# Kernel tuning notes

Measured on AMD Instinct MI355X. Metric: run time of the kernel, lower is better.

Reference implementation:

```python
import jax, jax.numpy as jnp
import numpy as np

NOT_EPSILON = 1.0
B, S, D = 1, 512, 256


def swishmax(x, axis):
    xexp = x * jnp.exp(x - jnp.max(x, axis=axis, keepdims=True))
    return xexp / (jnp.sum(jnp.abs(xexp), axis=axis, keepdims=True) + NOT_EPSILON)


def setup_inputs() -> dict:
    key = jax.random.key(0)
    ks = jax.random.split(key, 13)
    scale = 1.0 / np.sqrt(D)
    mk = lambda k: jax.random.uniform(k, (D, D), jnp.float32, -scale, scale)
    mb = lambda k: jax.random.uniform(k, (D,), jnp.float32, -scale, scale)
    return {
        "query_tokens": jax.random.normal(ks[0], (B, S, D), jnp.float32),
        "key_tokens": jax.random.normal(ks[1], (B, S, D), jnp.float32),
        "value_tokens": jax.random.normal(ks[2], (B, S, D), jnp.float32),
        "Wk": mk(ks[3]), "bk": mb(ks[4]),
        "Wq": mk(ks[5]), "bq": mb(ks[6]),
        "Wva": mk(ks[7]), "bva": mb(ks[8]),
        "Wl": mk(ks[9]), "bl": mb(ks[10]),
        "Wvo": mk(ks[11]), "bvo": mb(ks[12]),
    }


def reference(query_tokens, key_tokens, value_tokens,
              Wk, bk, Wq, bq, Wva, bva, Wl, bl, Wvo, bvo):
    # residual linear transforms of tokens
    k = key_tokens + key_tokens @ Wk + bk        # [B,S,D]
    q = query_tokens + query_tokens @ Wq + bq    # [B,S,D]
    # batchify: key -> [B,Sk,1,D], query -> [B,1,Sq,D]; outer-product scores
    attention_raw = k[:, :, None, :] * q[:, None, :, :]          # [B,Sk,Sq,D]
    attention_logits = attention_raw + attention_raw @ Wl + bl   # DxD linear on raw scores
    attention_scale = swishmax(attention_logits, axis=-2)        # normalize over query axis (dim -shape_dims)
    v = value_tokens + value_tokens @ Wva + bva  # [B,S,D]
    values_scaled = v[:, :, None, :] * attention_scale           # [B,Sk,Sq,D]
    value_sum = values_scaled.sum(axis=-3)                       # reduce key axis -> [B,Sq,D]
    value_out = value_sum + value_sum @ Wvo + bvo
    return value_out
```

## Files before the change

kernel.cpp:

```cpp
#include <hip/hip_runtime.h>
#include <math.h>

#define S_LEN 512
#define D_DIM 256
#define SLICE (S_LEN * D_DIM)

#define LOG2E  1.44269504088896f
#define LN2    0.69314718055995f
#define C2     (8.0f * LOG2E)

#define EXP2F(x) __builtin_amdgcn_exp2f(x)


typedef _Float16 half8  __attribute__((ext_vector_type(8)));
typedef _Float16 half4v __attribute__((ext_vector_type(4)));
typedef float   floatx4 __attribute__((ext_vector_type(4)));

__global__ __launch_bounds__(256) void linres3(
    const float* __restrict__ xk, const float* __restrict__ Wk,
    const float* __restrict__ bk, _Float16* __restrict__ yk16,
    const float* __restrict__ xq, const float* __restrict__ Wq,
    const float* __restrict__ bq, _Float16* __restrict__ yq16,
    const float* __restrict__ xv, const float* __restrict__ Wv,
    const float* __restrict__ bv, float* __restrict__ yv,
    const float* __restrict__ Wl, _Float16* __restrict__ WlhT)
{
    const int tid = threadIdx.x;
    const int sel = blockIdx.y;

    if (sel == 3) {
        #pragma unroll
        for (int t = 0; t < 2; ++t) {
            const int d = blockIdx.x * 2 + t;
            float v = (Wl[tid * D_DIM + d] + (tid == d ? 1.0f : 0.0f)) * LOG2E;
            WlhT[d * D_DIM + tid] = (_Float16)v;
        }
        return;
    }

    __shared__ float xs[4][D_DIM];
    const int r0 = blockIdx.x * 4;
    const float* x = sel == 0 ? xk : (sel == 1 ? xq : xv);
    const float* W = sel == 0 ? Wk : (sel == 1 ? Wq : Wv);
    const float* b = sel == 0 ? bk : (sel == 1 ? bq : bv);

    #pragma unroll
    for (int t = 0; t < 4; ++t) xs[t][tid] = x[(r0 + t) * D_DIM + tid];
    __syncthreads();
    const float bv_ = b[tid];
    float acc[4];
    #pragma unroll
    for (int i = 0; i < 4; ++i) acc[i] = xs[i][tid] + bv_;
    #pragma unroll 8
    for (int e = 0; e < D_DIM; ++e) {
        const float w = W[e * D_DIM + tid];
        #pragma unroll
        for (int i = 0; i < 4; ++i) acc[i] += xs[i][e] * w;
    }
    if (sel == 2) {
        #pragma unroll
        for (int i = 0; i < 4; ++i) yv[(r0 + i) * D_DIM + tid] = acc[i];
    } else {
        _Float16* y16 = sel == 0 ? yk16 : yq16;
        #pragma unroll
        for (int i = 0; i < 4; ++i) y16[(r0 + i) * D_DIM + tid] = (_Float16)acc[i];
    }
}

__global__ __launch_bounds__(256) void linres_sum(
    const float* __restrict__ po, const float* __restrict__ W,
    const float* __restrict__ b, float* __restrict__ y)
{
    __shared__ float xs[2][D_DIM];
    const int tid = threadIdx.x;
    const int r0  = blockIdx.x * 2;
    #pragma unroll
    for (int t = 0; t < 2; ++t) {
        float s = 0.f;
        #pragma unroll
        for (int c = 0; c < 16; ++c)
            s += po[(size_t)c * SLICE + (r0 + t) * D_DIM + tid];
        xs[t][tid] = s;
    }
    __syncthreads();
    const float bv_ = b[tid];
    float acc[2];
    #pragma unroll
    for (int i = 0; i < 2; ++i) acc[i] = xs[i][tid] + bv_;
    #pragma unroll 8
    for (int e = 0; e < D_DIM; ++e) {
        const float w = W[e * D_DIM + tid];
        #pragma unroll
        for (int i = 0; i < 2; ++i) acc[i] += xs[i][e] * w;
    }
    #pragma unroll
    for (int i = 0; i < 2; ++i) y[(r0 + i) * D_DIM + tid] = acc[i];
}

__device__ __forceinline__ void stage_q(const _Float16* __restrict__ qh,
                                        _Float16* __restrict__ Afrag,
                                        int sq0, int tid)
{
    const int i   = tid & 63;
    const int qtr = tid >> 6;
    const int mt = i >> 4, l16 = i & 15;
    const half8* src = (const half8*)(qh + (size_t)(sq0 + i) * D_DIM + qtr * 64);
    #pragma unroll
    for (int u = 0; u < 8; ++u) {
        const int eb   = qtr * 8 + u;
        const int kk   = eb >> 2, quad = eb & 3;
        const int addr16 = (mt * 8 + kk) * 64 + quad * 16 + l16;
        *(half8*)(Afrag + addr16 * 8) = src[u];
    }
}

__device__ __forceinline__ void stage_q32(const _Float16* __restrict__ qh,
                                          _Float16* __restrict__ Afrag,
                                          int sq0, int tid)
{
    const int i   = tid & 31;
    const int oct = tid >> 5;
    const int mt = i >> 4, l16 = i & 15;
    const half8* src = (const half8*)(qh + (size_t)(sq0 + i) * D_DIM);
    #pragma unroll
    for (int u = 0; u < 4; ++u) {
        const int eb   = oct * 4 + u;
        const int kk   = eb >> 2, quad = eb & 3;
        const int addr16 = (mt * 8 + kk) * 64 + quad * 16 + l16;
        *(half8*)(Afrag + addr16 * 8) = src[eb];
    }
}

__global__ __launch_bounds__(256, 2) void stats_mfma(
    const _Float16* __restrict__ qh, const _Float16* __restrict__ kh,
    const _Float16* __restrict__ WlhT, const float* __restrict__ bl,
    float* __restrict__ pm, float* __restrict__ ps)
{
    __shared__ _Float16 Afrag[32 * 64 * 8];

    const int tid  = threadIdx.x;
    const int lane = tid & 63, wave = tid >> 6;
    const int quad = lane >> 4, l16 = lane & 15;
    const int sqt  = blockIdx.x, sq0 = sqt * 64;
    const int dw   = blockIdx.y * 128 + wave * 32;
    const int sk0  = blockIdx.z * 16;

    stage_q(qh, Afrag, sq0, tid);

    half8 wl[2][8];
    #pragma unroll
    for (int nt = 0; nt < 2; ++nt) {
        const int d = dw + nt * 16 + l16;
        #pragma unroll
        for (int kk = 0; kk < 8; ++kk)
            wl[nt][kk] = *(const half8*)(WlhT + (size_t)d * D_DIM + kk * 32 + quad * 8);
    }
    float bl_r[2];
    #pragma unroll
    for (int nt = 0; nt < 2; ++nt)
        bl_r[nt] = bl[dw + nt * 16 + l16] * LOG2E;

    __syncthreads();

    #pragma unroll 1
    for (int s = 0; s < 16; ++s) {
        const int sk = sk0 + s;
        floatx4 acc[4][2];
        #pragma unroll
        for (int mt = 0; mt < 4; ++mt)
            #pragma unroll
            for (int nt = 0; nt < 2; ++nt)
                acc[mt][nt] = (floatx4){0.f, 0.f, 0.f, 0.f};

        #pragma unroll
        for (int kk = 0; kk < 8; ++kk) {
            const half8 k8 = *(const half8*)(kh + (size_t)sk * D_DIM + kk * 32 + quad * 8);
            half8 af[4], bf[2];
            #pragma unroll
            for (int mt = 0; mt < 4; ++mt)
                af[mt] = *(const half8*)(Afrag + ((mt * 8 + kk) * 64 + lane) * 8);
            #pragma unroll
            for (int nt = 0; nt < 2; ++nt)
                bf[nt] = wl[nt][kk] * k8;
            #pragma unroll
            for (int mt = 0; mt < 4; ++mt)
                #pragma unroll
                for (int nt = 0; nt < 2; ++nt)
                    acc[mt][nt] = __builtin_amdgcn_mfma_f32_16x16x32_f16(
                        af[mt], bf[nt], acc[mt][nt], 0, 0, 0);
        }

        #pragma unroll
        for (int nt = 0; nt < 2; ++nt) {
            float mmx[4], tss[4];
            #pragma unroll
            for (int mt = 0; mt < 4; ++mt) {
                float L0 = acc[mt][nt][0] + bl_r[nt];
                float L1 = acc[mt][nt][1] + bl_r[nt];
                float L2 = acc[mt][nt][2] + bl_r[nt];
                float L3 = acc[mt][nt][3] + bl_r[nt];
                float t0 = fabsf(L0) * EXP2F(L0 - C2);
                float t1 = fabsf(L1) * EXP2F(L1 - C2);
                float t2 = fabsf(L2) * EXP2F(L2 - C2);
                float t3 = fabsf(L3) * EXP2F(L3 - C2);
                mmx[mt] = fmaxf(fmaxf(L0, L1), fmaxf(L2, L3));
                tss[mt] = (t0 + t1) + (t2 + t3);
            }
            float m  = fmaxf(fmaxf(mmx[0], mmx[1]), fmaxf(mmx[2], mmx[3]));
            float ss = (tss[0] + tss[1]) + (tss[2] + tss[3]);

            #pragma unroll
            for (int mask = 16; mask <= 32; mask <<= 1) {
                m  = fmaxf(m, __shfl_xor(m, mask, 64));
                ss += __shfl_xor(ss, mask, 64);
            }
            if (quad == 0) {
                const int d = dw + nt * 16 + l16;
                pm[((size_t)sqt * S_LEN + sk) * D_DIM + d] = m;
                ps[((size_t)sqt * S_LEN + sk) * D_DIM + d] = ss;
            }
        }
    }
}

__global__ __launch_bounds__(256) void reduce_ms(
    const float* __restrict__ pm, const float* __restrict__ ps,
    const float* __restrict__ vbuf, float* __restrict__ wbuf)
{
    const int idx = blockIdx.x * 256 + threadIdx.x;
    float mv[8], sv[8];
    #pragma unroll
    for (int t = 0; t < 8; ++t) {
        mv[t] = pm[(size_t)t * SLICE + idx];
        sv[t] = ps[(size_t)t * SLICE + idx];
    }
    float M = fmaxf(fmaxf(fmaxf(mv[0], mv[1]), fmaxf(mv[2], mv[3])),
                    fmaxf(fmaxf(mv[4], mv[5]), fmaxf(mv[6], mv[7])));
    float S = ((sv[0] + sv[1]) + (sv[2] + sv[3]))
            + ((sv[4] + sv[5]) + (sv[6] + sv[7]));
    const float denom = S * LN2 + EXP2F(M - C2);
    wbuf[idx] = vbuf[idx] * (LN2 / denom);
}

__global__ __launch_bounds__(256)
__attribute__((amdgpu_waves_per_eu(2, 2)))
void accum_mfma(
    const _Float16* __restrict__ qh, const _Float16* __restrict__ kh,
    const _Float16* __restrict__ WlhT, const float* __restrict__ bl,
    const float* __restrict__ wbuf, float* __restrict__ po)
{
    __shared__ _Float16 Afrag[16 * 64 * 8];

    const int tid  = threadIdx.x;
    const int lane = tid & 63, wave = tid >> 6;
    const int quad = lane >> 4, l16 = lane & 15;
    const int sq0  = blockIdx.x * 32;
    const int dw   = blockIdx.y * 128 + wave * 32;
    const int chunk = blockIdx.z;
    const int sk0  = chunk * 32;

    stage_q32(qh, Afrag, sq0, tid);

    half8 wl[2][8];
    #pragma unroll
    for (int nt = 0; nt < 2; ++nt) {
        const int d = dw + nt * 16 + l16;
        #pragma unroll
        for (int kk = 0; kk < 8; ++kk)
            wl[nt][kk] = *(const half8*)(WlhT + (size_t)d * D_DIM + kk * 32 + quad * 8);
    }
    float bl_r[2];
    #pragma unroll
    for (int nt = 0; nt < 2; ++nt)
        bl_r[nt] = bl[dw + nt * 16 + l16] * LOG2E;

    __syncthreads();

    half8 afr[2][8];
    #pragma unroll
    for (int mt = 0; mt < 2; ++mt)
        #pragma unroll
        for (int kk = 0; kk < 8; ++kk)
            afr[mt][kk] = *(const half8*)(Afrag + ((mt * 8 + kk) * 64 + lane) * 8);

    floatx4 o[2][2];
    #pragma unroll
    for (int mt = 0; mt < 2; ++mt)
        #pragma unroll
        for (int nt = 0; nt < 2; ++nt)
            o[mt][nt] = (floatx4){0.f, 0.f, 0.f, 0.f};

    half8 k8c[8];
    #pragma unroll
    for (int kk = 0; kk < 8; ++kk)
        k8c[kk] = *(const half8*)(kh + (size_t)sk0 * D_DIM + kk * 32 + quad * 8);
    float w_c0 = wbuf[(size_t)sk0 * D_DIM + dw + l16];
    float w_c1 = wbuf[(size_t)sk0 * D_DIM + dw + 16 + l16];

    #pragma unroll 1
    for (int s = 0; s < 32; ++s) {
        const int sk = sk0 + s;

        floatx4 acc[2][2];
        #pragma unroll
        for (int mt = 0; mt < 2; ++mt)
            #pragma unroll
            for (int nt = 0; nt < 2; ++nt)
                acc[mt][nt] = (floatx4){0.f, 0.f, 0.f, 0.f};

        #pragma unroll
        for (int kk = 0; kk < 8; ++kk) {
            const half8 bf0 = wl[0][kk] * k8c[kk];
            const half8 bf1 = wl[1][kk] * k8c[kk];
            acc[0][0] = __builtin_amdgcn_mfma_f32_16x16x32_f16(afr[0][kk], bf0, acc[0][0], 0, 0, 0);
            acc[0][1] = __builtin_amdgcn_mfma_f32_16x16x32_f16(afr[0][kk], bf1, acc[0][1], 0, 0, 0);
            acc[1][0] = __builtin_amdgcn_mfma_f32_16x16x32_f16(afr[1][kk], bf0, acc[1][0], 0, 0, 0);
            acc[1][1] = __builtin_amdgcn_mfma_f32_16x16x32_f16(afr[1][kk], bf1, acc[1][1], 0, 0, 0);
        }

        const float w_use0 = w_c0, w_use1 = w_c1;
        if (s < 31) {
            #pragma unroll
            for (int kk = 0; kk < 8; ++kk)
                k8c[kk] = *(const half8*)(kh + (size_t)(sk + 1) * D_DIM + kk * 32 + quad * 8);
            w_c0 = wbuf[(size_t)(sk + 1) * D_DIM + dw + l16];
            w_c1 = wbuf[(size_t)(sk + 1) * D_DIM + dw + 16 + l16];
        }

        #pragma unroll
        for (int mt = 0; mt < 2; ++mt)
            #pragma unroll
            for (int r = 0; r < 4; ++r) {
                const float La = acc[mt][0][r] + bl_r[0];
                const float Lb = acc[mt][1][r] + bl_r[1];
                o[mt][0][r] += w_use0 * (La * EXP2F(La - C2));
                o[mt][1][r] += w_use1 * (Lb * EXP2F(Lb - C2));
            }
    }

    float* dst = po + (size_t)chunk * SLICE;
    #pragma unroll
    for (int mt = 0; mt < 2; ++mt)
        #pragma unroll
        for (int nt = 0; nt < 2; ++nt)
            #pragma unroll
            for (int r = 0; r < 4; ++r) {
                const int row = sq0 + mt * 16 + quad * 4 + r;
                const int col = dw + nt * 16 + l16;
                dst[(size_t)row * D_DIM + col] = o[mt][nt][r];
            }
}

extern "C" void kernel_launch(void* const* d_in, const int* in_sizes, int n_in,
                              void* d_out, int out_size, void* d_ws, size_t ws_size,
                              hipStream_t stream)
{
    const float* query = (const float*)d_in[0];
    const float* key   = (const float*)d_in[1];
    const float* value = (const float*)d_in[2];
    const float* Wk  = (const float*)d_in[3];
    const float* bk  = (const float*)d_in[4];
    const float* Wq  = (const float*)d_in[5];
    const float* bq  = (const float*)d_in[6];
    const float* Wva = (const float*)d_in[7];
    const float* bva = (const float*)d_in[8];
    const float* Wl  = (const float*)d_in[9];
    const float* bl  = (const float*)d_in[10];
    const float* Wvo = (const float*)d_in[11];
    const float* bvo = (const float*)d_in[12];

    const int MAT = SLICE;
    float* ws   = (float*)d_ws;
    float* vbuf = ws + 2 * MAT;
    float* wbuf = ws + 3 * MAT;
    _Float16* WlhT = (_Float16*)(ws + 6 * MAT);
    _Float16* kh   = (_Float16*)(ws + 6 * MAT + 32768);
    _Float16* qh   = kh + MAT;
    float* pm  = ws + 6 * MAT + 32768 + 2 * 65536;
    float* ps  = pm + 8 * MAT;
    float* po  = pm;
    float* out = (float*)d_out;

    linres3<<<dim3(128, 4), 256, 0, stream>>>(key, Wk, bk, kh,
                                              query, Wq, bq, qh,
                                              value, Wva, bva, vbuf,
                                              Wl, WlhT);

    stats_mfma<<<dim3(8, 2, 32), 256, 0, stream>>>(qh, kh, WlhT, bl, pm, ps);
    reduce_ms<<<512, 256, 0, stream>>>(pm, ps, vbuf, wbuf);
    accum_mfma<<<dim3(16, 2, 16), 256, 0, stream>>>(qh, kh, WlhT, bl,
                                                    wbuf, po);

    linres_sum<<<256, 256, 0, stream>>>(po, Wvo, bvo, out);
}
```

Measured before the change: 194.5 us.

## Fuse all five kernels into one persistent kernel with grid barriers

Replaces the five separate launches (linear projections, stats, reduce, accumulate, output projection) with a single 512-block kernel that runs each phase in turn and separates them with a software grid-wide barrier built on atomics. The aim is to remove per-launch overhead and the gaps between kernels. The price is that every phase must now use 512 blocks, the shared-memory buffer is the largest one needed by any phase, and the final projection is done one row per block. All 512 blocks must be resident at once or the barrier deadlocks, and barrier spinning adds its own latency.

```diff
diff --git a/kernel.cpp b/kernel.cpp
--- a/kernel.cpp
+++ b/kernel.cpp
@@ -4,6 +4,7 @@
 #define S_LEN 512
 #define D_DIM 256
 #define SLICE (S_LEN * D_DIM)
+#define NBLK  512
 
 #define LOG2E  1.44269504088896f
 #define LN2    0.69314718055995f
@@ -13,342 +14,346 @@
 
 
 typedef _Float16 half8  __attribute__((ext_vector_type(8)));
-typedef _Float16 half4v __attribute__((ext_vector_type(4)));
 typedef float   floatx4 __attribute__((ext_vector_type(4)));
 
-__global__ __launch_bounds__(256) void linres3(
-    const float* __restrict__ xk, const float* __restrict__ Wk,
-    const float* __restrict__ bk, _Float16* __restrict__ yk16,
-    const float* __restrict__ xq, const float* __restrict__ Wq,
-    const float* __restrict__ bq, _Float16* __restrict__ yq16,
-    const float* __restrict__ xv, const float* __restrict__ Wv,
-    const float* __restrict__ bv, float* __restrict__ yv,
-    const float* __restrict__ Wl, _Float16* __restrict__ WlhT)
+__device__ __forceinline__ void grid_barrier(int* bar)
 {
-    const int tid = threadIdx.x;
-    const int sel = blockIdx.y;
-
-    if (sel == 3) {
-        #pragma unroll
-        for (int t = 0; t < 2; ++t) {
-            const int d = blockIdx.x * 2 + t;
-            float v = (Wl[tid * D_DIM + d] + (tid == d ? 1.0f : 0.0f)) * LOG2E;
-            WlhT[d * D_DIM + tid] = (_Float16)v;
-        }
-        return;
-    }
-
-    __shared__ float xs[4][D_DIM];
-    const int r0 = blockIdx.x * 4;
-    const float* x = sel == 0 ? xk : (sel == 1 ? xq : xv);
-    const float* W = sel == 0 ? Wk : (sel == 1 ? Wq : Wv);
-    const float* b = sel == 0 ? bk : (sel == 1 ? bq : bv);
-
-    #pragma unroll
-    for (int t = 0; t < 4; ++t) xs[t][tid] = x[(r0 + t) * D_DIM + tid];
     __syncthreads();
-    const float bv_ = b[tid];
-    float acc[4];
-    #pragma unroll
-    for (int i = 0; i < 4; ++i) acc[i] = xs[i][tid] + bv_;
-    #pragma unroll 8
-    for (int e = 0; e < D_DIM; ++e) {
-        const float w = W[e * D_DIM + tid];
-        #pragma unroll
-        for (int i = 0; i < 4; ++i) acc[i] += xs[i][e] * w;
-    }
-    if (sel == 2) {
-        #pragma unroll
-        for (int i = 0; i < 4; ++i) yv[(r0 + i) * D_DIM + tid] = acc[i];
-    } else {
-        _Float16* y16 = sel == 0 ? yk16 : yq16;
-        #pragma unroll
-        for (int i = 0; i < 4; ++i) y16[(r0 + i) * D_DIM + tid] = (_Float16)acc[i];
-    }
+    if (threadIdx.x == 0) {
+        __threadfence();
+        int* cnt = bar;
+        int* gen = bar + 1;
+        const int g = __hip_atomic_load(gen, __ATOMIC_RELAXED,
+                                        __HIP_MEMORY_SCOPE_AGENT);
+        const int prev = __hip_atomic_fetch_add(cnt, 1, __ATOMIC_ACQ_REL,
+                                                __HIP_MEMORY_SCOPE_AGENT);
+        if (prev == NBLK - 1) {
+            __hip_atomic_store(cnt, 0, __ATOMIC_RELAXED,
+                               __HIP_MEMORY_SCOPE_AGENT);
+            __hip_atomic_fetch_add(gen, 1, __ATOMIC_RELEASE,
+                                   __HIP_MEMORY_SCOPE_AGENT);
+        } else {
+            while (__hip_atomic_load(gen, __ATOMIC_RELAXED,
+                                     __HIP_MEMORY_SCOPE_AGENT) == g)
+                __builtin_amdgcn_s_sleep(8);
+        }
+        __threadfence();
+    }
+    __syncthreads();
 }
 
-__global__ __launch_bounds__(256) void linres_sum(
-    const float* __restrict__ po, const float* __restrict__ W,
-    const float* __restrict__ b, float* __restrict__ y)
+__global__ __launch_bounds__(256)
+__attribute__((amdgpu_waves_per_eu(2, 2)))
+void fused_all(
+    const float* __restrict__ query, const float* __restrict__ key,
+    const float* __restrict__ value,
+    const float* __restrict__ Wk,  const float* __restrict__ bk,
+    const float* __restrict__ Wq,  const float* __restrict__ bq,
+    const float* __restrict__ Wva, const float* __restrict__ bva,
+    const float* __restrict__ Wl,  const float* __restrict__ bl,
+    const float* __restrict__ Wvo, const float* __restrict__ bvo,
+    _Float16* __restrict__ kh, _Float16* __restrict__ qh,
+    float* __restrict__ vbuf, _Float16* __restrict__ WlhT,
+    float* __restrict__ pm, float* __restrict__ ps,
+    float* __restrict__ wbuf, float* __restrict__ po,
+    float* __restrict__ out, int* bar)
 {
-    __shared__ float xs[2][D_DIM];
-    const int tid = threadIdx.x;
-    const int r0  = blockIdx.x * 2;
-    #pragma unroll
-    for (int t = 0; t < 2; ++t) {
-        float s = 0.f;
-        #pragma unroll
-        for (int c = 0; c < 16; ++c)
-            s += po[(size_t)c * SLICE + (r0 + t) * D_DIM + tid];
-        xs[t][tid] = s;
-    }
-    __syncthreads();
-    const float bv_ = b[tid];
-    float acc[2];
-    #pragma unroll
-    for (int i = 0; i < 2; ++i) acc[i] = xs[i][tid] + bv_;
-    #pragma unroll 8
-    for (int e = 0; e < D_DIM; ++e) {
-        const float w = W[e * D_DIM + tid];
-        #pragma unroll
-        for (int i = 0; i < 2; ++i) acc[i] += xs[i][e] * w;
-    }
-    #pragma unroll
-    for (int i = 0; i < 2; ++i) y[(r0 + i) * D_DIM + tid] = acc[i];
-}
-
-__device__ __forceinline__ void stage_q(const _Float16* __restrict__ qh,
-                                        _Float16* __restrict__ Afrag,
-                                        int sq0, int tid)
-{
-    const int i   = tid & 63;
-    const int qtr = tid >> 6;
-    const int mt = i >> 4, l16 = i & 15;
-    const half8* src = (const half8*)(qh + (size_t)(sq0 + i) * D_DIM + qtr * 64);
-    #pragma unroll
-    for (int u = 0; u < 8; ++u) {
-        const int eb   = qtr * 8 + u;
-        const int kk   = eb >> 2, quad = eb & 3;
-        const int addr16 = (mt * 8 + kk) * 64 + quad * 16 + l16;
-        *(half8*)(Afrag + addr16 * 8) = src[u];
-    }
-}
-
-__device__ __forceinline__ void stage_q32(const _Float16* __restrict__ qh,
-                                          _Float16* __restrict__ Afrag,
-                                          int sq0, int tid)
-{
-    const int i   = tid & 31;
-    const int oct = tid >> 5;
-    const int mt = i >> 4, l16 = i & 15;
-    const half8* src = (const half8*)(qh + (size_t)(sq0 + i) * D_DIM);
-    #pragma unroll
-    for (int u = 0; u < 4; ++u) {
-        const int eb   = oct * 4 + u;
-        const int kk   = eb >> 2, quad = eb & 3;
-        const int addr16 = (mt * 8 + kk) * 64 + quad * 16 + l16;
-        *(half8*)(Afrag + addr16 * 8) = src[eb];
-    }
-}
-
-__global__ __launch_bounds__(256, 2) void stats_mfma(
-    const _Float16* __restrict__ qh, const _Float16* __restrict__ kh,
-    const _Float16* __restrict__ WlhT, const float* __restrict__ bl,
-    float* __restrict__ pm, float* __restrict__ ps)
-{
-    __shared__ _Float16 Afrag[32 * 64 * 8];
+    __shared__ __align__(16) _Float16 AfragS[32 * 64 * 8];
 
     const int tid  = threadIdx.x;
+    const int bid  = blockIdx.x;
     const int lane = tid & 63, wave = tid >> 6;
     const int quad = lane >> 4, l16 = lane & 15;
-    const int sqt  = blockIdx.x, sq0 = sqt * 64;
-    const int dw   = blockIdx.y * 128 + wave * 32;
-    const int sk0  = blockIdx.z * 16;
-
-    stage_q(qh, Afrag, sq0, tid);
-
-    half8 wl[2][8];
-    #pragma unroll
-    for (int nt = 0; nt < 2; ++nt) {
-        const int d = dw + nt * 16 + l16;
+
+    {
+        const int sel = bid >> 7;
+        const int bx  = bid & 127;
+        if (sel == 3) {
+            #pragma unroll
+            for (int t = 0; t < 2; ++t) {
+                const int d = bx * 2 + t;
+                float v = (Wl[tid * D_DIM + d] + (tid == d ? 1.0f : 0.0f)) * LOG2E;
+                WlhT[d * D_DIM + tid] = (_Float16)v;
+            }
+        } else {
+            float* xsf = (float*)AfragS;
+            const int r0 = bx * 4;
+            const float* x = sel == 0 ? key : (sel == 1 ? query : value);
+            const float* W = sel == 0 ? Wk : (sel == 1 ? Wq : Wva);
+            const float* b = sel == 0 ? bk : (sel == 1 ? bq : bva);
+
+            #pragma unroll
+            for (int t = 0; t < 4; ++t)
+                xsf[t * D_DIM + tid] = x[(r0 + t) * D_DIM + tid];
+            __syncthreads();
+            const float bv_ = b[tid];
+            float acc[4];
+            #pragma unroll
+            for (int i = 0; i < 4; ++i) acc[i] = xsf[i * D_DIM + tid] + bv_;
+            #pragma unroll 8
+            for (int e = 0; e < D_DIM; ++e) {
+                const float w = W[e * D_DIM + tid];
+                #pragma unroll
+                for (int i = 0; i < 4; ++i) acc[i] += xsf[i * D_DIM + e] * w;
+            }
+            if (sel == 2) {
+                #pragma unroll
+                for (int i = 0; i < 4; ++i) vbuf[(r0 + i) * D_DIM + tid] = acc[i];
+            } else {
+                _Float16* y16 = sel == 0 ? kh : qh;
+                #pragma unroll
+                for (int i = 0; i < 4; ++i)
+                    y16[(r0 + i) * D_DIM + tid] = (_Float16)acc[i];
+            }
+        }
+    }
+    grid_barrier(bar);
+
+    {
+        _Float16* Afrag = AfragS;
+        const int sqt = bid & 7,  sq0 = sqt * 64;
+        const int by  = (bid >> 3) & 1;
+        const int bz  = bid >> 4;
+        const int dw  = by * 128 + wave * 32;
+        const int sk0 = bz * 16;
+
+        {
+            const int i   = tid & 63;
+            const int qtr = tid >> 6;
+            const int mt = i >> 4, sl16 = i & 15;
+            const half8* src = (const half8*)(qh + (size_t)(sq0 + i) * D_DIM + qtr * 64);
+            #pragma unroll
+            for (int u = 0; u < 8; ++u) {
+                const int eb = qtr * 8 + u;
+                const int kk = eb >> 2, q4 = eb & 3;
+                const int addr16 = (mt * 8 + kk) * 64 + q4 * 16 + sl16;
+                *(half8*)(Afrag + addr16 * 8) = src[u];
+            }
+        }
+
+        half8 wl[2][8];
+        #pragma unroll
+        for (int nt = 0; nt < 2; ++nt) {
+            const int d = dw + nt * 16 + l16;
+            #pragma unroll
+            for (int kk = 0; kk < 8; ++kk)
+                wl[nt][kk] = *(const half8*)(WlhT + (size_t)d * D_DIM + kk * 32 + quad * 8);
+        }
+        float bl_r[2];
+        #pragma unroll
+        for (int nt = 0; nt < 2; ++nt)
+            bl_r[nt] = bl[dw + nt * 16 + l16] * LOG2E;
+
+        __syncthreads();
+
+        #pragma unroll 1
+        for (int s = 0; s < 16; ++s) {
+            const int sk = sk0 + s;
+            floatx4 acc[4][2];
+            #pragma unroll
+            for (int mt = 0; mt < 4; ++mt)
+                #pragma unroll
+                for (int nt = 0; nt < 2; ++nt)
+                    acc[mt][nt] = (floatx4){0.f, 0.f, 0.f, 0.f};
+
+            #pragma unroll
+            for (int kk = 0; kk < 8; ++kk) {
+                const half8 k8 = *(const half8*)(kh + (size_t)sk * D_DIM + kk * 32 + quad * 8);
+                half8 af[4], bf[2];
+                #pragma unroll
+                for (int mt = 0; mt < 4; ++mt)
+                    af[mt] = *(const half8*)(Afrag + ((mt * 8 + kk) * 64 + lane) * 8);
+                #pragma unroll
+                for (int nt = 0; nt < 2; ++nt)
+                    bf[nt] = wl[nt][kk] * k8;
+                #pragma unroll
+                for (int mt = 0; mt < 4; ++mt)
+                    #pragma unroll
+                    for (int nt = 0; nt < 2; ++nt)
+                        acc[mt][nt] = __builtin_amdgcn_mfma_f32_16x16x32_f16(
+                            af[mt], bf[nt], acc[mt][nt], 0, 0, 0);
+            }
+
+            #pragma unroll
+            for (int nt = 0; nt < 2; ++nt) {
+                float mmx[4], tss[4];
+                #pragma unroll
+                for (int mt = 0; mt < 4; ++mt) {
+                    float L0 = acc[mt][nt][0] + bl_r[nt];
+                    float L1 = acc[mt][nt][1] + bl_r[nt];
+                    float L2 = acc[mt][nt][2] + bl_r[nt];
+                    float L3 = acc[mt][nt][3] + bl_r[nt];
+                    float t0 = fabsf(L0) * EXP2F(L0 - C2);
+                    float t1 = fabsf(L1) * EXP2F(L1 - C2);
+                    float t2 = fabsf(L2) * EXP2F(L2 - C2);
+                    float t3 = fabsf(L3) * EXP2F(L3 - C2);
+                    mmx[mt] = fmaxf(fmaxf(L0, L1), fmaxf(L2, L3));
+                    tss[mt] = (t0 + t1) + (t2 + t3);
+                }
+                float m  = fmaxf(fmaxf(mmx[0], mmx[1]), fmaxf(mmx[2], mmx[3]));
+                float ss = (tss[0] + tss[1]) + (tss[2] + tss[3]);
+
+                #pragma unroll
+                for (int mask = 16; mask <= 32; mask <<= 1) {
+                    m  = fmaxf(m, __shfl_xor(m, mask, 64));
+                    ss += __shfl_xor(ss, mask, 64);
+                }
+                if (quad == 0) {
+                    const int d = dw + nt * 16 + l16;
+                    pm[((size_t)sqt * S_LEN + sk) * D_DIM + d] = m;
+                    ps[((size_t)sqt * S_LEN + sk) * D_DIM + d] = ss;
+                }
+            }
+        }
+    }
+    grid_barrier(bar);
+
+    {
+        const int idx = bid * 256 + tid;
+        float mv[8], sv[8];
+        #pragma unroll
+        for (int t = 0; t < 8; ++t) {
+            mv[t] = pm[(size_t)t * SLICE + idx];
+            sv[t] = ps[(size_t)t * SLICE + idx];
+        }
+        float M = fmaxf(fmaxf(fmaxf(mv[0], mv[1]), fmaxf(mv[2], mv[3])),
+                        fmaxf(fmaxf(mv[4], mv[5]), fmaxf(mv[6], mv[7])));
+        float S = ((sv[0] + sv[1]) + (sv[2] + sv[3]))
+                + ((sv[4] + sv[5]) + (sv[6] + sv[7]));
+        const float denom = S * LN2 + EXP2F(M - C2);
+        wbuf[idx] = vbuf[idx] * (LN2 / denom);
+    }
+    grid_barrier(bar);
+
+    {
+        _Float16* Afrag = AfragS;
+        const int bx = bid & 15;
+        const int by = (bid >> 4) & 1;
+        const int chunk = bid >> 5;
+        const int sq0 = bx * 32;
+        const int dw  = by * 128 + wave * 32;
+        const int sk0 = chunk * 32;
+
+        {
+            const int i   = tid & 31;
+            const int oct = tid >> 5;
+            const int mt = i >> 4, sl16 = i & 15;
+            const half8* src = (const half8*)(qh + (size_t)(sq0 + i) * D_DIM);
+            #pragma unroll
+            for (int u = 0; u < 4; ++u) {
+                const int eb = oct * 4 + u;
+                const int kk = eb >> 2, q4 = eb & 3;
+                const int addr16 = (mt * 8 + kk) * 64 + q4 * 16 + sl16;
+                *(half8*)(Afrag + addr16 * 8) = src[eb];
+            }
+        }
+
+        half8 wl[2][8];
+        #pragma unroll
+        for (int nt = 0; nt < 2; ++nt) {
+            const int d = dw + nt * 16 + l16;
+            #pragma unroll
+            for (int kk = 0; kk < 8; ++kk)
+                wl[nt][kk] = *(const half8*)(WlhT + (size_t)d * D_DIM + kk * 32 + quad * 8);
+        }
+        float bl_r[2];
+        #pragma unroll
+        for (int nt = 0; nt < 2; ++nt)
+            bl_r[nt] = bl[dw + nt * 16 + l16] * LOG2E;
+
+        __syncthreads();
+
+        half8 afr[2][8];
+        #pragma unroll
+        for (int mt = 0; mt < 2; ++mt)
+            #pragma unroll
+            for (int kk = 0; kk < 8; ++kk)
+                afr[mt][kk] = *(const half8*)(Afrag + ((mt * 8 + kk) * 64 + lane) * 8);
+
+        floatx4 o[2][2];
+        #pragma unroll
+        for (int mt = 0; mt < 2; ++mt)
+            #pragma unroll
+            for (int nt = 0; nt < 2; ++nt)
+                o[mt][nt] = (floatx4){0.f, 0.f, 0.f, 0.f};
+
+        half8 k8c[8];
         #pragma unroll
         for (int kk = 0; kk < 8; ++kk)
-            wl[nt][kk] = *(const half8*)(WlhT + (size_t)d * D_DIM + kk * 32 + quad * 8);
-    }
-    float bl_r[2];
-    #pragma unroll
-    for (int nt = 0; nt < 2; ++nt)
-        bl_r[nt] = bl[dw + nt * 16 + l16] * LOG2E;
-
-    __syncthreads();
-
-    #pragma unroll 1
-    for (int s = 0; s < 16; ++s) {
-        const int sk = sk0 + s;
-        floatx4 acc[4][2];
-        #pragma unroll
-        for (int mt = 0; mt < 4; ++mt)
+            k8c[kk] = *(const half8*)(kh + (size_t)sk0 * D_DIM + kk * 32 + quad * 8);
+        float w_c0 = wbuf[(size_t)sk0 * D_DIM + dw + l16];
+        float w_c1 = wbuf[(size_t)sk0 * D_DIM + dw + 16 + l16];
+
+        #pragma unroll 1
+        for (int s = 0; s < 32; ++s) {
+            const int sk = sk0 + s;
+
+            floatx4 acc[2][2];
+            #pragma unroll
+            for (int mt = 0; mt < 2; ++mt)
+                #pragma unroll
+                for (int nt = 0; nt < 2; ++nt)
+                    acc[mt][nt] = (floatx4){0.f, 0.f, 0.f, 0.f};
+
+            #pragma unroll
+            for (int kk = 0; kk < 8; ++kk) {
+                const half8 bf0 = wl[0][kk] * k8c[kk];
+                const half8 bf1 = wl[1][kk] * k8c[kk];
+                acc[0][0] = __builtin_amdgcn_mfma_f32_16x16x32_f16(afr[0][kk], bf0, acc[0][0], 0, 0, 0);
+                acc[0][1] = __builtin_amdgcn_mfma_f32_16x16x32_f16(afr[0][kk], bf1, acc[0][1], 0, 0, 0);
+                acc[1][0] = __builtin_amdgcn_mfma_f32_16x16x32_f16(afr[1][kk], bf0, acc[1][0], 0, 0, 0);
+                acc[1][1] = __builtin_amdgcn_mfma_f32_16x16x32_f16(afr[1][kk], bf1, acc[1][1], 0, 0, 0);
+            }
+
+            const float w_use0 = w_c0, w_use1 = w_c1;
+            if (s < 31) {
+                #pragma unroll
+                for (int kk = 0; kk < 8; ++kk)
+                    k8c[kk] = *(const half8*)(kh + (size_t)(sk + 1) * D_DIM + kk * 32 + quad * 8);
+                w_c0 = wbuf[(size_t)(sk + 1) * D_DIM + dw + l16];
+                w_c1 = wbuf[(size_t)(sk + 1) * D_DIM + dw + 16 + l16];
+            }
+
+            #pragma unroll
+            for (int mt = 0; mt < 2; ++mt)
+                #pragma unroll
+                for (int r = 0; r < 4; ++r) {
+                    const float La = acc[mt][0][r] + bl_r[0];
+                    const float Lb = acc[mt][1][r] + bl_r[1];
+                    o[mt][0][r] += w_use0 * (La * EXP2F(La - C2));
+                    o[mt][1][r] += w_use1 * (Lb * EXP2F(Lb - C2));
+                }
+        }
+
+        float* dst = po + (size_t)chunk * SLICE;
+        #pragma unroll
+        for (int mt = 0; mt < 2; ++mt)
             #pragma unroll
             for (int nt = 0; nt < 2; ++nt)
-                acc[mt][nt] = (floatx4){0.f, 0.f, 0.f, 0.f};
-
-        #pragma unroll
-        for (int kk = 0; kk < 8; ++kk) {
-            const half8 k8 = *(const half8*)(kh + (size_t)sk * D_DIM + kk * 32 + quad * 8);
-            half8 af[4], bf[2];
-            #pragma unroll
-            for (int mt = 0; mt < 4; ++mt)
-                af[mt] = *(const half8*)(Afrag + ((mt * 8 + kk) * 64 + lane) * 8);
-            #pragma unroll
-            for (int nt = 0; nt < 2; ++nt)
-                bf[nt] = wl[nt][kk] * k8;
-            #pragma unroll
-            for (int mt = 0; mt < 4; ++mt)
-                #pragma unroll
-                for (int nt = 0; nt < 2; ++nt)
-                    acc[mt][nt] = __builtin_amdgcn_mfma_f32_16x16x32_f16(
-                        af[mt], bf[nt], acc[mt][nt], 0, 0, 0);
-        }
-
-        #pragma unroll
-        for (int nt = 0; nt < 2; ++nt) {
-            float mmx[4], tss[4];
-            #pragma unroll
-            for (int mt = 0; mt < 4; ++mt) {
-                float L0 = acc[mt][nt][0] + bl_r[nt];
-                float L1 = acc[mt][nt][1] + bl_r[nt];
-                float L2 = acc[mt][nt][2] + bl_r[nt];
-                float L3 = acc[mt][nt][3] + bl_r[nt];
-                float t0 = fabsf(L0) * EXP2F(L0 - C2);
-                float t1 = fabsf(L1) * EXP2F(L1 - C2);
-                float t2 = fabsf(L2) * EXP2F(L2 - C2);
-                float t3 = fabsf(L3) * EXP2F(L3 - C2);
-                mmx[mt] = fmaxf(fmaxf(L0, L1), fmaxf(L2, L3));
-                tss[mt] = (t0 + t1) + (t2 + t3);
-            }
-            float m  = fmaxf(fmaxf(mmx[0], mmx[1]), fmaxf(mmx[2], mmx[3]));
-            float ss = (tss[0] + tss[1]) + (tss[2] + tss[3]);
-
-            #pragma unroll
-            for (int mask = 16; mask <= 32; mask <<= 1) {
-                m  = fmaxf(m, __shfl_xor(m, mask, 64));
-                ss += __shfl_xor(ss, mask, 64);
-            }
-            if (quad == 0) {
-                const int d = dw + nt * 16 + l16;
-                pm[((size_t)sqt * S_LEN + sk) * D_DIM + d] = m;
-                ps[((size_t)sqt * S_LEN + sk) * D_DIM + d] = ss;
-            }
-        }
-    }
-}
-
-__global__ __launch_bounds__(256) void reduce_ms(
-    const float* __restrict__ pm, const float* __restrict__ ps,
-    const float* __restrict__ vbuf, float* __restrict__ wbuf)
-{
-    const int idx = blockIdx.x * 256 + threadIdx.x;
-    float mv[8], sv[8];
-    #pragma unroll
-    for (int t = 0; t < 8; ++t) {
-        mv[t] = pm[(size_t)t * SLICE + idx];
-        sv[t] = ps[(size_t)t * SLICE + idx];
-    }
-    float M = fmaxf(fmaxf(fmaxf(mv[0], mv[1]), fmaxf(mv[2], mv[3])),
-                    fmaxf(fmaxf(mv[4], mv[5]), fmaxf(mv[6], mv[7])));
-    float S = ((sv[0] + sv[1]) + (sv[2] + sv[3]))
-            + ((sv[4] + sv[5]) + (sv[6] + sv[7]));
-    const float denom = S * LN2 + EXP2F(M - C2);
-    wbuf[idx] = vbuf[idx] * (LN2 / denom);
-}
-
-__global__ __launch_bounds__(256)
-__attribute__((amdgpu_waves_per_eu(2, 2)))
-void accum_mfma(
-    const _Float16* __restrict__ qh, const _Float16* __restrict__ kh,
-    const _Float16* __restrict__ WlhT, const float* __restrict__ bl,
-    const float* __restrict__ wbuf, float* __restrict__ po)
-{
-    __shared__ _Float16 Afrag[16 * 64 * 8];
-
-    const int tid  = threadIdx.x;
-    const int lane = tid & 63, wave = tid >> 6;
-    const int quad = lane >> 4, l16 = lane & 15;
-    const int sq0  = blockIdx.x * 32;
-    const int dw   = blockIdx.y * 128 + wave * 32;
-    const int chunk = blockIdx.z;
-    const int sk0  = chunk * 32;
-
-    stage_q32(qh, Afrag, sq0, tid);
-
-    half8 wl[2][8];
-    #pragma unroll
-    for (int nt = 0; nt < 2; ++nt) {
-        const int d = dw + nt * 16 + l16;
-        #pragma unroll
-        for (int kk = 0; kk < 8; ++kk)
-            wl[nt][kk] = *(const half8*)(WlhT + (size_t)d * D_DIM + kk * 32 + quad * 8);
-    }
-    float bl_r[2];
-    #pragma unroll
-    for (int nt = 0; nt < 2; ++nt)
-        bl_r[nt] = bl[dw + nt * 16 + l16] * LOG2E;
-
-    __syncthreads();
-
-    half8 afr[2][8];
-    #pragma unroll
-    for (int mt = 0; mt < 2; ++mt)
-        #pragma unroll
-        for (int kk = 0; kk < 8; ++kk)
-            afr[mt][kk] = *(const half8*)(Afrag + ((mt * 8 + kk) * 64 + lane) * 8);
-
-    floatx4 o[2][2];
-    #pragma unroll
-    for (int mt = 0; mt < 2; ++mt)
-        #pragma unroll
-        for (int nt = 0; nt < 2; ++nt)
-            o[mt][nt] = (floatx4){0.f, 0.f, 0.f, 0.f};
-
-    half8 k8c[8];
-    #pragma unroll
-    for (int kk = 0; kk < 8; ++kk)
-        k8c[kk] = *(const half8*)(kh + (size_t)sk0 * D_DIM + kk * 32 + quad * 8);
-    float w_c0 = wbuf[(size_t)sk0 * D_DIM + dw + l16];
-    float w_c1 = wbuf[(size_t)sk0 * D_DIM + dw + 16 + l16];
-
-    #pragma unroll 1
-    for (int s = 0; s < 32; ++s) {
-        const int sk = sk0 + s;
-
-        floatx4 acc[2][2];
-        #pragma unroll
-        for (int mt = 0; mt < 2; ++mt)
-            #pragma unroll
-            for (int nt = 0; nt < 2; ++nt)
-                acc[mt][nt] = (floatx4){0.f, 0.f, 0.f, 0.f};
-
-        #pragma unroll
-        for (int kk = 0; kk < 8; ++kk) {
-            const half8 bf0 = wl[0][kk] * k8c[kk];
-            const half8 bf1 = wl[1][kk] * k8c[kk];
-            acc[0][0] = __builtin_amdgcn_mfma_f32_16x16x32_f16(afr[0][kk], bf0, acc[0][0], 0, 0, 0);
-            acc[0][1] = __builtin_amdgcn_mfma_f32_16x16x32_f16(afr[0][kk], bf1, acc[0][1], 0, 0, 0);
-            acc[1][0] = __builtin_amdgcn_mfma_f32_16x16x32_f16(afr[1][kk], bf0, acc[1][0], 0, 0, 0);
-            acc[1][1] = __builtin_amdgcn_mfma_f32_16x16x32_f16(afr[1][kk], bf1, acc[1][1], 0, 0, 0);
-        }
-
-        const float w_use0 = w_c0, w_use1 = w_c1;
-        if (s < 31) {
-            #pragma unroll
-            for (int kk = 0; kk < 8; ++kk)
-                k8c[kk] = *(const half8*)(kh + (size_t)(sk + 1) * D_DIM + kk * 32 + quad * 8);
-            w_c0 = wbuf[(size_t)(sk + 1) * D_DIM + dw + l16];
-            w_c1 = wbuf[(size_t)(sk + 1) * D_DIM + dw + 16 + l16];
-        }
-
-        #pragma unroll
-        for (int mt = 0; mt < 2; ++mt)
-            #pragma unroll
-            for (int r = 0; r < 4; ++r) {
-                const float La = acc[mt][0][r] + bl_r[0];
-                const float Lb = acc[mt][1][r] + bl_r[1];
-                o[mt][0][r] += w_use0 * (La * EXP2F(La - C2));
-                o[mt][1][r] += w_use1 * (Lb * EXP2F(Lb - C2));
-            }
-    }
-
-    float* dst = po + (size_t)chunk * SLICE;
-    #pragma unroll
-    for (int mt = 0; mt < 2; ++mt)
-        #pragma unroll
-        for (int nt = 0; nt < 2; ++nt)
-            #pragma unroll
-            for (int r = 0; r < 4; ++r) {
-                const int row = sq0 + mt * 16 + quad * 4 + r;
-                const int col = dw + nt * 16 + l16;
-                dst[(size_t)row * D_DIM + col] = o[mt][nt][r];
-            }
+                #pragma unroll
+                for (int r = 0; r < 4; ++r) {
+                    const int row = sq0 + mt * 16 + quad * 4 + r;
+                    const int col = dw + nt * 16 + l16;
+                    dst[(size_t)row * D_DIM + col] = o[mt][nt][r];
+                }
+    }
+    grid_barrier(bar);
+
+    {
+        float* xs = (float*)AfragS;
+        const int r0 = bid;
+        float s = 0.f;
+        #pragma unroll
+        for (int c = 0; c < 16; ++c)
+            s += po[(size_t)c * SLICE + (size_t)r0 * D_DIM + tid];
+        xs[tid] = s;
+        __syncthreads();
+        float acc = s + bvo[tid];
+        #pragma unroll 8
+        for (int e = 0; e < D_DIM; ++e)
+            acc += xs[e] * Wvo[e * D_DIM + tid];
+        out[(size_t)r0 * D_DIM + tid] = acc;
+    }
 }
 
 extern "C" void kernel_launch(void* const* d_in, const int* in_sizes, int n_in,
@@ -371,6 +376,7 @@
 
     const int MAT = SLICE;
     float* ws   = (float*)d_ws;
+    int*   bar  = (int*)ws;
     float* vbuf = ws + 2 * MAT;
     float* wbuf = ws + 3 * MAT;
     _Float16* WlhT = (_Float16*)(ws + 6 * MAT);
@@ -381,15 +387,8 @@
     float* po  = pm;
     float* out = (float*)d_out;
 
-    linres3<<<dim3(128, 4), 256, 0, stream>>>(key, Wk, bk, kh,
-                                              query, Wq, bq, qh,
-                                              value, Wva, bva, vbuf,
-                                              Wl, WlhT);
-
-    stats_mfma<<<dim3(8, 2, 32), 256, 0, stream>>>(qh, kh, WlhT, bl, pm, ps);
-    reduce_ms<<<512, 256, 0, stream>>>(pm, ps, vbuf, wbuf);
-    accum_mfma<<<dim3(16, 2, 16), 256, 0, stream>>>(qh, kh, WlhT, bl,
-                                                    wbuf, po);
-
-    linres_sum<<<256, 256, 0, stream>>>(po, Wvo, bvo, out);
+    hipMemsetAsync(bar, 0, 2 * sizeof(int), stream);
+    fused_all<<<dim3(NBLK), dim3(256), 0, stream>>>(
+        query, key, value, Wk, bk, Wq, bq, Wva, bva, Wl, bl, Wvo, bvo,
+        kh, qh, vbuf, WlhT, pm, ps, wbuf, po, out, bar);
 }
```

Measured after the change: 466.2 us. 140% more time.
